# Kernel tuning notes

Measured on AMD Instinct MI355X. Metric: run time of the kernel, lower is better.

The kernel has to match this reference:

```python
import jax, jax.numpy as jnp
import numpy as np

B, P, N, H = 8, 12, 5000, 8
E = 50000
NB = 8
TD0, TD1 = 16, 64
MAX_STEPS = 500


def _proj(x, w1, b1, w2, b2):
    # Projection: Linear -> ReLU -> Linear
    return jax.nn.relu(x @ w1 + b1) @ w2 + b2


def _ln(x, w, b, eps=1e-5):
    # LayerNorm over last two dims [N, H] with affine params [N, H]
    m = jnp.mean(x, axis=(-2, -1), keepdims=True)
    v = jnp.mean((x - m) ** 2, axis=(-2, -1), keepdims=True)
    return (x - m) * jax.lax.rsqrt(v + eps) * w + b


def _time_table():
    # DiffTimeEmbedding buffer: [MAX_STEPS, 2*TD0]
    steps = jnp.arange(MAX_STEPS, dtype=jnp.float32)[:, None]
    dims = jnp.arange(TD0, dtype=jnp.float32)[None, :]
    e = steps * 10.0 ** (dims * 4.0 / TD0)
    return jnp.concatenate([jnp.sin(e), jnp.cos(e)], axis=1)


def setup_inputs() -> dict:
    key = jax.random.key(0)
    ks = jax.random.split(key, 40)
    rn = lambda k, s, sc=0.1: jax.random.normal(k, s, jnp.float32) * sc
    return {
        'x': jax.random.normal(ks[0], (B, P, N), jnp.float32),
        'cond': jax.random.normal(ks[1], (B, P, N, H), jnp.float32),
        'pos': jax.random.normal(ks[2], (N, H), jnp.float32),
        'time': jax.random.randint(ks[3], (B,), 0, MAX_STEPS),
        'edge_index': jax.random.randint(ks[4], (2, E), 0, N),
        'te_w1': rn(ks[5], (2 * TD0, TD1)), 'te_b1': rn(ks[6], (TD1,)),
        'te_w2': rn(ks[7], (TD1, TD1)), 'te_b2': rn(ks[8], (TD1,)),
        'in_w1': rn(ks[9], (1, H)), 'in_b1': rn(ks[10], (H,)),
        'in_w2': rn(ks[11], (H, H)), 'in_b2': rn(ks[12], (H,)),
        'pos_w1': rn(ks[13], (H, H)), 'pos_b1': rn(ks[14], (H,)),
        'pos_w2': rn(ks[15], (H, H)), 'pos_b2': rn(ks[16], (H,)),
        'attn': jax.random.normal(ks[17], (NB + 1, 1), jnp.float32),
        'bt_w1': rn(ks[18], (NB, TD1, H)), 'bt_b1': rn(ks[19], (NB, H)),
        'bt_w2': rn(ks[20], (NB, H, H)), 'bt_b2': rn(ks[21], (NB, H)),
        'bc_w1': rn(ks[22], (NB, H, H)), 'bc_b1': rn(ks[23], (NB, H)),
        'bc_w2': rn(ks[24], (NB, H, H)), 'bc_b2': rn(ks[25], (NB, H)),
        'gn_w': 1.0 + rn(ks[26], (NB, N, H), 0.05), 'gn_b': rn(ks[27], (NB, N, H), 0.05),
        'tn_w': 1.0 + rn(ks[28], (NB, N, H), 0.05), 'tn_b': rn(ks[29], (NB, N, H), 0.05),
        'cv_w': rn(ks[30], (NB, P, P)), 'cv_b': rn(ks[31], (NB, P)),
        'out_w1': rn(ks[32], (H, H)), 'out_b1': rn(ks[33], (H,)),
        'out_w2': rn(ks[34], (H, 1)), 'out_b2': rn(ks[35], (1,)),
    }


def _forward(x, cond, pos, te_w1, te_b1, te_w2, te_b2, in_w1, in_b1, in_w2, in_b2,
             pos_w1, pos_b1, pos_w2, pos_b2, attn, bt_w1, bt_b1, bt_w2, bt_b2,
             bc_w1, bc_b1, bc_w2, bc_b2, gn_w, gn_b, tn_w, tn_b, cv_w, cv_b,
             out_w1, out_b1, out_w2, out_b2, time, edge_index):
    # diffusion-time embedding -> [B, TD1]
    te = _time_table()[time]
    te = jax.nn.silu(te @ te_w1 + te_b1)
    te = jax.nn.silu(te @ te_w2 + te_b2)
    # input + positional projection -> [B, P, N, H]
    h = _proj(x[..., None], in_w1, in_b1, in_w2, in_b2)
    h = h + _proj(pos, pos_w1, pos_b1, pos_w2, pos_b2)
    # LGConv symmetric GCN norm (no self loops), shared across blocks
    src, dst = edge_index[0], edge_index[1]
    deg = jnp.zeros((N,), h.dtype).at[dst].add(1.0)
    dinv = jnp.where(deg > 0, 1.0 / jnp.sqrt(jnp.where(deg > 0, deg, 1.0)), 0.0)
    enorm = dinv[src] * dinv[dst]  # [E]
    skips = [h]
    for i in range(NB):
        t = _proj(te, bt_w1[i], bt_b1[i], bt_w2[i], bt_b2[i])[:, None, None, :]
        c = _proj(cond, bc_w1[i], bc_b1[i], bc_w2[i], bc_b2[i])
        h = _ln(h + c, gn_w[i], gn_b[i])
        # LGConv: gather -> scale -> scatter-add along node dim (-2)
        msg = h[:, :, src, :] * enorm[None, None, :, None]
        h = jnp.zeros_like(h).at[:, :, dst, :].add(msg)
        h = _ln(h + t, tn_w[i], tn_b[i])
        # 1x1 Conv2d over period channels
        h = jnp.einsum('bpnh,qp->bqnh', h, cv_w[i]) + cv_b[i][None, :, None, None]
        skips.append(h)
    s = jnp.stack(skips, axis=-1)  # [B, P, N, H, NB+1]
    a = jax.nn.softmax(attn, axis=0)  # [NB+1, 1]
    h = (s @ a)[..., 0]  # [B, P, N, H]
    return _proj(h, out_w1, out_b1, out_w2, out_b2)[..., 0]  # [B, P, N]


def reference(x, cond, pos, te_w1, te_b1, te_w2, te_b2, in_w1, in_b1, in_w2, in_b2,
              pos_w1, pos_b1, pos_w2, pos_b2, attn, bt_w1, bt_b1, bt_w2, bt_b2,
              bc_w1, bc_b1, bc_w2, bc_b2, gn_w, gn_b, tn_w, tn_b, cv_w, cv_b,
              out_w1, out_b1, out_w2, out_b2, time, edge_index):
    return _forward(x, cond, pos, te_w1, te_b1, te_w2, te_b2, in_w1, in_b1, in_w2, in_b2,
                    pos_w1, pos_b1, pos_w2, pos_b2, attn, bt_w1, bt_b1, bt_w2, bt_b2,
                    bc_w1, bc_b1, bc_w2, bc_b2, gn_w, gn_b, tn_w, tn_b, cv_w, cv_b,
                    out_w1, out_b1, out_w2, out_b2, time, edge_index)
```

## Files before the change

### kernel.cpp

```cpp
#include <hip/hip_runtime.h>
#include <math.h>

#define Bv 8
#define Pv 12
#define Nv 5000
#define Hv 8
#define Ev 50000
#define NBv 8
#define TD1v 64
#define NIMG (Bv * Pv)
#define BLKS_PER_IMG 20

__device__ __constant__ float POW10Q[16] = {
  1.0f, 1.7782794100389228f, 3.1622776601683795f, 5.623413251903491f,
  10.0f, 17.78279410038923f, 31.622776601683793f, 56.23413251903491f,
  100.0f, 177.82794100389228f, 316.22776601683796f, 562.341325190349f,
  1000.0f, 1778.2794100389228f, 3162.2776601683795f, 5623.413251903491f
};

__global__ void k_setup(const int* timei, const float* attn,
                        const float* te_w1, const float* te_b1,
                        const float* te_w2, const float* te_b2,
                        const float* bt_w1, const float* bt_b1,
                        const float* bt_w2, const float* bt_b2,
                        float* t_all, float* a9) {
  __shared__ float te0[Bv][32];
  __shared__ float te1[Bv][64];
  __shared__ float te2[Bv][64];
  int t = threadIdx.x;
  for (int idx = t; idx < Bv * 16; idx += 64) {
    int b = idx >> 4, d = idx & 15;
    float e = (float)timei[b] * POW10Q[d];
    te0[b][d]      = (float)sin((double)e);
    te0[b][d + 16] = (float)cos((double)e);
  }
  __syncthreads();
  for (int idx = t; idx < Bv * 64; idx += 64) {
    int b = idx >> 6, j = idx & 63;
    float s = te_b1[j];
    for (int k = 0; k < 32; ++k) s += te0[b][k] * te_w1[k * 64 + j];
    te1[b][j] = s / (1.0f + expf(-s));
  }
  __syncthreads();
  for (int idx = t; idx < Bv * 64; idx += 64) {
    int b = idx >> 6, j = idx & 63;
    float s = te_b2[j];
    for (int k = 0; k < 64; ++k) s += te1[b][k] * te_w2[k * 64 + j];
    te2[b][j] = s / (1.0f + expf(-s));
  }
  __syncthreads();
  {
    int i = t >> 3, b = t & 7;
    float u[Hv];
    for (int j = 0; j < Hv; ++j) {
      float s = bt_b1[i * Hv + j];
      for (int k = 0; k < TD1v; ++k) s += te2[b][k] * bt_w1[(i * TD1v + k) * Hv + j];
      u[j] = fmaxf(s, 0.0f);
    }
    for (int ch = 0; ch < Hv; ++ch) {
      float s = bt_b2[i * Hv + ch];
      for (int j = 0; j < Hv; ++j) s += u[j] * bt_w2[(i * Hv + j) * Hv + ch];
      t_all[(i * Bv + b) * Hv + ch] = s;
    }
  }
  if (t == 0) {
    float m = attn[0];
    for (int i = 1; i < 9; ++i) m = fmaxf(m, attn[i]);
    float s = 0.f, ex[9];
    for (int i = 0; i < 9; ++i) { ex[i] = expf(attn[i] - m); s += ex[i]; }
    for (int i = 0; i < 9; ++i) a9[i] = ex[i] / s;
  }
}

__global__ void k_posp(const float* pos, const float* pw1, const float* pb1,
                       const float* pw2, const float* pb2, float* posp) {
  int n = blockIdx.x * blockDim.x + threadIdx.x;
  if (n >= Nv) return;
  const float4* pr = (const float4*)(pos + (size_t)n * Hv);
  float4 r0 = pr[0], r1 = pr[1];
  float x[8] = {r0.x, r0.y, r0.z, r0.w, r1.x, r1.y, r1.z, r1.w};
  float u[8];
  #pragma unroll
  for (int j = 0; j < 8; ++j) {
    float s = pb1[j];
    #pragma unroll
    for (int k = 0; k < 8; ++k) s += x[k] * pw1[k * 8 + j];
    u[j] = fmaxf(s, 0.f);
  }
  float o[8];
  #pragma unroll
  for (int ch = 0; ch < 8; ++ch) {
    float s = pb2[ch];
    #pragma unroll
    for (int j = 0; j < 8; ++j) s += u[j] * pw2[j * 8 + ch];
    o[ch] = s;
  }
  float4* po = (float4*)(posp + (size_t)n * Hv);
  po[0] = make_float4(o[0], o[1], o[2], o[3]);
  po[1] = make_float4(o[4], o[5], o[6], o[7]);
}

__global__ void k_zero(float* deg, int* cursor, float* stats) {
  int i = blockIdx.x * blockDim.x + threadIdx.x;
  if (i < Nv) { deg[i] = 0.f; cursor[i] = 0; }
  if (i < NBv * 2 * NIMG * 2) stats[i] = 0.f;
}

__global__ void k_deg(const int* eidx, float* deg) {
  int e = blockIdx.x * blockDim.x + threadIdx.x;
  if (e < Ev) atomicAdd(&deg[eidx[Ev + e]], 1.0f);
}

__global__ void k_dinv(const float* deg, float* dinv) {
  int n = blockIdx.x * blockDim.x + threadIdx.x;
  if (n < Nv) {
    float d = deg[n];
    dinv[n] = d > 0.f ? (float)(1.0 / sqrt((double)d)) : 0.f;
  }
}

__global__ void k_scan(const float* deg, int* row_ptr) {
  __shared__ int buf[1024];
  __shared__ int base_s;
  int t = threadIdx.x;
  if (t == 0) { base_s = 0; row_ptr[0] = 0; }
  __syncthreads();
  for (int c = 0; c < 5; ++c) {
    int i = c * 1024 + t;
    int v = (i < Nv) ? (int)(deg[i] + 0.5f) : 0;
    buf[t] = v;
    __syncthreads();
    for (int off = 1; off < 1024; off <<= 1) {
      int add = (t >= off) ? buf[t - off] : 0;
      __syncthreads();
      buf[t] += add;
      __syncthreads();
    }
    int base = base_s;
    if (i < Nv) row_ptr[i + 1] = base + buf[t];
    __syncthreads();
    if (t == 1023) base_s = base + buf[1023];
    __syncthreads();
  }
}

__global__ void k_csr(const int* eidx, const float* dinv, const int* row_ptr,
                      int* cursor, float2* epack) {
  int e = blockIdx.x * blockDim.x + threadIdx.x;
  if (e >= Ev) return;
  int s = eidx[e], d = eidx[Ev + e];
  int slot = atomicAdd(&cursor[d], 1);
  int pos = row_ptr[d] + slot;
  epack[pos] = make_float2(__int_as_float(s), dinv[s] * dinv[d]);
}

__global__ __launch_bounds__(256) void k_gwb(
    const int* __restrict__ row_ptr, const float2* __restrict__ epack,
    const float* __restrict__ gn_w, const float* __restrict__ gn_b,
    float* __restrict__ Gw, float* __restrict__ Gb) {
  int id = blockIdx.x * 256 + threadIdx.x;
  if (id >= NBv * Nv) return;
  int i = id / Nv, n = id % Nv;
  const float* gw = gn_w + (size_t)i * Nv * Hv;
  const float* gb = gn_b + (size_t)i * Nv * Hv;
  float aw[8] = {0,0,0,0,0,0,0,0}, ab[8] = {0,0,0,0,0,0,0,0};
  int e0 = row_ptr[n], e1 = row_ptr[n + 1];
  for (int e = e0; e < e1; ++e) {
    float2 ep = epack[e];
    int s = __float_as_int(ep.x);
    float w = ep.y;
    const float4* wr = (const float4*)(gw + (size_t)s * Hv);
    const float4* br = (const float4*)(gb + (size_t)s * Hv);
    float4 w0 = wr[0], w1 = wr[1], b0 = br[0], b1 = br[1];
    aw[0] += w * w0.x; aw[1] += w * w0.y; aw[2] += w * w0.z; aw[3] += w * w0.w;
    aw[4] += w * w1.x; aw[5] += w * w1.y; aw[6] += w * w1.z; aw[7] += w * w1.w;
    ab[0] += w * b0.x; ab[1] += w * b0.y; ab[2] += w * b0.z; ab[3] += w * b0.w;
    ab[4] += w * b1.x; ab[5] += w * b1.y; ab[6] += w * b1.z; ab[7] += w * b1.w;
  }
  float4* wo = (float4*)(Gw + (size_t)id * Hv);
  wo[0] = make_float4(aw[0], aw[1], aw[2], aw[3]);
  wo[1] = make_float4(aw[4], aw[5], aw[6], aw[7]);
  float4* bo = (float4*)(Gb + (size_t)id * Hv);
  bo[0] = make_float4(ab[0], ab[1], ab[2], ab[3]);
  bo[1] = make_float4(ab[4], ab[5], ab[6], ab[7]);
}

__global__ void k_init(const float* x, const float* posp,
                       const float* iw1, const float* ib1,
                       const float* iw2, const float* ib2,
                       const float* a9, float* hA, float* acc) {
  int t = blockIdx.x * blockDim.x + threadIdx.x;
  if (t >= Bv * Pv * Nv) return;
  float xv = x[t];
  float u[8];
  #pragma unroll
  for (int j = 0; j < 8; ++j) u[j] = fmaxf(xv * iw1[j] + ib1[j], 0.f);
  int n = t % Nv;
  const float4* pp = (const float4*)(posp + (size_t)n * Hv);
  float4 p0 = pp[0], p1 = pp[1];
  float pv[8] = {p0.x, p0.y, p0.z, p0.w, p1.x, p1.y, p1.z, p1.w};
  float a0 = a9[0];
  float o[8];
  #pragma unroll
  for (int ch = 0; ch < 8; ++ch) {
    float s = ib2[ch];
    #pragma unroll
    for (int j = 0; j < 8; ++j) s += u[j] * iw2[j * 8 + ch];
    o[ch] = s + pv[ch];
  }
  float4* hr = (float4*)(hA + (size_t)t * Hv);
  hr[0] = make_float4(o[0], o[1], o[2], o[3]);
  hr[1] = make_float4(o[4], o[5], o[6], o[7]);
  float4* ar = (float4*)(acc + (size_t)t * Hv);
  ar[0] = make_float4(a0 * o[0], a0 * o[1], a0 * o[2], a0 * o[3]);
  ar[1] = make_float4(a0 * o[4], a0 * o[5], a0 * o[6], a0 * o[7]);
}

__device__ inline void partial_to_stats(float s1, float s2, float* stats_g) {
  #pragma unroll
  for (int off = 32; off > 0; off >>= 1) {
    s1 += __shfl_down(s1, off, 64);
    s2 += __shfl_down(s2, off, 64);
  }
  __shared__ float r1[4], r2[4];
  int wid = threadIdx.x >> 6, lane = threadIdx.x & 63;
  if (lane == 0) { r1[wid] = s1; r2[wid] = s2; }
  __syncthreads();
  if (threadIdx.x == 0) {
    float a = r1[0] + r1[1] + r1[2] + r1[3];
    float b = r2[0] + r2[1] + r2[2] + r2[3];
    atomicAdd(&stats_g[0], a);
    atomicAdd(&stats_g[1], b);
  }
}

__device__ inline void img_swizzle(int bx, int& g, int& chunk) {
  int xcd = bx & 7;
  int local = bx >> 3;
  g = xcd * 12 + local / BLKS_PER_IMG;
  chunk = local % BLKS_PER_IMG;
}

__global__ __launch_bounds__(256) void k_stage1(
    const float* __restrict__ h, const float* __restrict__ cond,
    const float* w1, const float* b1, const float* w2, const float* b2,
    const float* __restrict__ gnw,
    float* __restrict__ vt, float* stats1) {
  __shared__ float lw1[64], lw2[64], lb1[8], lb2[8];
  int t = threadIdx.x;
  if (t < 64) lw1[t] = w1[t];
  else if (t < 128) lw2[t - 64] = w2[t - 64];
  else if (t < 136) lb1[t - 128] = b1[t - 128];
  else if (t < 144) lb2[t - 136] = b2[t - 136];
  __syncthreads();
  int g, chunk;
  img_swizzle(blockIdx.x, g, chunk);
  int n = chunk * 256 + t;
  float s1 = 0.f, s2 = 0.f;
  if (n < Nv) {
    size_t row = ((size_t)g * Nv + n) * Hv;
    const float4* cr = (const float4*)(cond + row);
    float4 c0 = cr[0], c1 = cr[1];
    float xc[8] = {c0.x, c0.y, c0.z, c0.w, c1.x, c1.y, c1.z, c1.w};
    float u[8];
    #pragma unroll
    for (int j = 0; j < 8; ++j) {
      float s = lb1[j];
      #pragma unroll
      for (int k = 0; k < 8; ++k) s += xc[k] * lw1[k * 8 + j];
      u[j] = fmaxf(s, 0.f);
    }
    const float4* hr = (const float4*)(h + row);
    float4 h0 = hr[0], h1 = hr[1];
    float hv[8] = {h0.x, h0.y, h0.z, h0.w, h1.x, h1.y, h1.z, h1.w};
    const float4* gr = (const float4*)(gnw + (size_t)n * Hv);
    float4 g0 = gr[0], g1 = gr[1];
    float gv[8] = {g0.x, g0.y, g0.z, g0.w, g1.x, g1.y, g1.z, g1.w};
    float o[8];
    #pragma unroll
    for (int ch = 0; ch < 8; ++ch) {
      float s = lb2[ch];
      #pragma unroll
      for (int j = 0; j < 8; ++j) s += u[j] * lw2[j * 8 + ch];
      float val = s + hv[ch];
      s1 += val; s2 += val * val;
      o[ch] = val * gv[ch];
    }
    float4* vo = (float4*)(vt + row);
    vo[0] = make_float4(o[0], o[1], o[2], o[3]);
    vo[1] = make_float4(o[4], o[5], o[6], o[7]);
  }
  partial_to_stats(s1, s2, stats1 + (size_t)g * 2);
}

__global__ __launch_bounds__(256) void k_stage2(
    const float* __restrict__ vt, float* __restrict__ v2,
    const int* __restrict__ row_ptr, const float2* __restrict__ epack,
    const float* __restrict__ Gw, const float* __restrict__ Gb,
    const float* __restrict__ stats1, float* stats2,
    const float* __restrict__ tvec) {
  int t = threadIdx.x;
  int g, chunk;
  img_swizzle(blockIdx.x, g, chunk);
  int n = chunk * 256 + t;
  int b = g / Pv;
  float mean = stats1[g * 2] * (1.f / 40000.f);
  float m2   = stats1[g * 2 + 1] * (1.f / 40000.f);
  float var  = m2 - mean * mean;
  float rstd = (float)(1.0 / sqrt((double)var + 1e-5));
  float mrs  = mean * rstd;
  float s1 = 0.f, s2 = 0.f;
  if (n < Nv) {
    size_t ibase = (size_t)g * Nv * Hv;
    float a8[8] = {0.f, 0.f, 0.f, 0.f, 0.f, 0.f, 0.f, 0.f};
    int e0 = row_ptr[n], e1 = row_ptr[n + 1];
    for (int e = e0; e < e1; ++e) {
      float2 ep = epack[e];
      int s = __float_as_int(ep.x);
      float w = ep.y;
      const float4* sr = (const float4*)(vt + ibase + (size_t)s * Hv);
      float4 x0 = sr[0], x1 = sr[1];
      a8[0] += w * x0.x; a8[1] += w * x0.y; a8[2] += w * x0.z; a8[3] += w * x0.w;
      a8[4] += w * x1.x; a8[5] += w * x1.y; a8[6] += w * x1.z; a8[7] += w * x1.w;
    }
    const float4* wr = (const float4*)(Gw + (size_t)n * Hv);
    const float4* br = (const float4*)(Gb + (size_t)n * Hv);
    float4 w0 = wr[0], w1 = wr[1], b0 = br[0], b1 = br[1];
    float gw8[8] = {w0.x, w0.y, w0.z, w0.w, w1.x, w1.y, w1.z, w1.w};
    float gb8[8] = {b0.x, b0.y, b0.z, b0.w, b1.x, b1.y, b1.z, b1.w};
    float o[8];
    #pragma unroll
    for (int ch = 0; ch < 8; ++ch) {
      float val = rstd * a8[ch] - mrs * gw8[ch] + gb8[ch] + tvec[b * Hv + ch];
      o[ch] = val;
      s1 += val; s2 += val * val;
    }
    float4* vo = (float4*)(v2 + ibase + (size_t)n * Hv);
    vo[0] = make_float4(o[0], o[1], o[2], o[3]);
    vo[1] = make_float4(o[4], o[5], o[6], o[7]);
  }
  partial_to_stats(s1, s2, stats2 + (size_t)g * 2);
}

__global__ __launch_bounds__(256) void k_stage3(
    float* __restrict__ v2, float* __restrict__ acc,
    const float* __restrict__ stats2,
    const float* __restrict__ tnw, const float* __restrict__ tnb,
    const float* __restrict__ cw, const float* __restrict__ cb,
    const float* __restrict__ a9, int iblk) {
  __shared__ float scw[144], scb[12], smean[12], srstd[12];
  int t = threadIdx.x;
  int b = blockIdx.x & 7;
  int chunk = blockIdx.x >> 3;
  if (t < 144) scw[t] = cw[t];
  else if (t < 156) scb[t - 144] = cb[t - 144];
  else if (t < 168) {
    int p = t - 156;
    int g = b * Pv + p;
    float mean = stats2[g * 2] * (1.f / 40000.f);
    float m2   = stats2[g * 2 + 1] * (1.f / 40000.f);
    float var  = m2 - mean * mean;
    smean[p] = mean;
    srstd[p] = (float)(1.0 / sqrt((double)var + 1e-5));
  }
  __syncthreads();
  int idx = chunk * 256 + t;
  if (idx >= Nv * 2) return;
  int n = idx >> 1, c4 = idx & 1;
  size_t noff = (size_t)n * Hv + c4 * 4;
  const float4 w4 = *(const float4*)(tnw + noff);
  const float4 b4 = *(const float4*)(tnb + noff);
  size_t strideP = (size_t)Nv * Hv;
  size_t base = (size_t)b * Pv * strideP + noff;
  float4 in[12];
  #pragma unroll
  for (int p = 0; p < 12; ++p) {
    float4 v = *(const float4*)(v2 + base + p * strideP);
    float mean = smean[p], rstd = srstd[p];
    in[p].x = (v.x - mean) * rstd * w4.x + b4.x;
    in[p].y = (v.y - mean) * rstd * w4.y + b4.y;
    in[p].z = (v.z - mean) * rstd * w4.z + b4.z;
    in[p].w = (v.w - mean) * rstd * w4.w + b4.w;
  }
  float ai = a9[iblk + 1];
  #pragma unroll
  for (int q = 0; q < 12; ++q) {
    float4 o = make_float4(scb[q], scb[q], scb[q], scb[q]);
    #pragma unroll
    for (int p = 0; p < 12; ++p) {
      float c = scw[q * 12 + p];
      o.x += c * in[p].x; o.y += c * in[p].y;
      o.z += c * in[p].z; o.w += c * in[p].w;
    }
    size_t off = base + q * strideP;
    *(float4*)(v2 + off) = o;
    float4* ap = (float4*)(acc + off);
    float4 av = *ap;
    av.x += ai * o.x; av.y += ai * o.y; av.z += ai * o.z; av.w += ai * o.w;
    *ap = av;
  }
}

__global__ void k_out(const float* acc, const float* ow1, const float* ob1,
                      const float* ow2, const float* ob2, float* out) {
  int t = blockIdx.x * blockDim.x + threadIdx.x;
  if (t >= Bv * Pv * Nv) return;
  const float4* ar = (const float4*)(acc + (size_t)t * Hv);
  float4 a0 = ar[0], a1 = ar[1];
  float x[8] = {a0.x, a0.y, a0.z, a0.w, a1.x, a1.y, a1.z, a1.w};
  float o = ob2[0];
  #pragma unroll
  for (int j = 0; j < 8; ++j) {
    float s = ob1[j];
    #pragma unroll
    for (int k = 0; k < 8; ++k) s += x[k] * ow1[k * 8 + j];
    o += fmaxf(s, 0.f) * ow2[j];
  }
  out[t] = o;
}

extern "C" void kernel_launch(void* const* d_in, const int* in_sizes, int n_in,
                              void* d_out, int out_size, void* d_ws, size_t ws_size,
                              hipStream_t stream) {
  const float* x      = (const float*)d_in[0];
  const float* cond   = (const float*)d_in[1];
  const float* pos    = (const float*)d_in[2];
  const int*   timei  = (const int*)  d_in[3];
  const int*   eidx   = (const int*)  d_in[4];
  const float* te_w1  = (const float*)d_in[5];
  const float* te_b1  = (const float*)d_in[6];
  const float* te_w2  = (const float*)d_in[7];
  const float* te_b2  = (const float*)d_in[8];
  const float* in_w1  = (const float*)d_in[9];
  const float* in_b1  = (const float*)d_in[10];
  const float* in_w2  = (const float*)d_in[11];
  const float* in_b2  = (const float*)d_in[12];
  const float* pos_w1 = (const float*)d_in[13];
  const float* pos_b1 = (const float*)d_in[14];
  const float* pos_w2 = (const float*)d_in[15];
  const float* pos_b2 = (const float*)d_in[16];
  const float* attn   = (const float*)d_in[17];
  const float* bt_w1  = (const float*)d_in[18];
  const float* bt_b1  = (const float*)d_in[19];
  const float* bt_w2  = (const float*)d_in[20];
  const float* bt_b2  = (const float*)d_in[21];
  const float* bc_w1  = (const float*)d_in[22];
  const float* bc_b1  = (const float*)d_in[23];
  const float* bc_w2  = (const float*)d_in[24];
  const float* bc_b2  = (const float*)d_in[25];
  const float* gn_w   = (const float*)d_in[26];
  const float* gn_b   = (const float*)d_in[27];
  const float* tn_w   = (const float*)d_in[28];
  const float* tn_b   = (const float*)d_in[29];
  const float* cv_w   = (const float*)d_in[30];
  const float* cv_b   = (const float*)d_in[31];
  const float* out_w1 = (const float*)d_in[32];
  const float* out_b1 = (const float*)d_in[33];
  const float* out_w2 = (const float*)d_in[34];
  const float* out_b2 = (const float*)d_in[35];
  float* out = (float*)d_out;

  const size_t HSZ = (size_t)Bv * Pv * Nv * Hv;
  float* ws    = (float*)d_ws;
  float* X     = ws;
  float* Y     = X + HSZ;
  float* acc   = Y + HSZ;
  float* posp  = acc + HSZ;
  float* deg   = posp + Nv * Hv;
  float* dinv  = deg + Nv;
  float* epack = dinv + Nv;
  float* t_all = epack + 2 * Ev;
  float* a9    = t_all + NBv * Bv * Hv;
  float* stats = a9 + 16;
  float* Gw    = stats + NBv * 2 * NIMG * 2;
  float* Gb    = Gw + NBv * Nv * Hv;
  int* row_ptr = (int*)(Gb + NBv * Nv * Hv);
  int* cursor  = row_ptr + Nv + 8;

  k_setup<<<1, 64, 0, stream>>>(timei, attn, te_w1, te_b1, te_w2, te_b2,
                                bt_w1, bt_b1, bt_w2, bt_b2, t_all, a9);
  k_posp<<<(Nv + 255) / 256, 256, 0, stream>>>(pos, pos_w1, pos_b1, pos_w2, pos_b2, posp);
  k_zero<<<(Nv + 255) / 256, 256, 0, stream>>>(deg, cursor, stats);
  k_deg<<<(Ev + 255) / 256, 256, 0, stream>>>(eidx, deg);
  k_dinv<<<(Nv + 255) / 256, 256, 0, stream>>>(deg, dinv);
  k_scan<<<1, 1024, 0, stream>>>(deg, row_ptr);
  k_csr<<<(Ev + 255) / 256, 256, 0, stream>>>(eidx, dinv, row_ptr, cursor, (float2*)epack);
  k_gwb<<<(NBv * Nv + 255) / 256, 256, 0, stream>>>(
      row_ptr, (const float2*)epack, gn_w, gn_b, Gw, Gb);
  k_init<<<(Bv * Pv * Nv + 255) / 256, 256, 0, stream>>>(
      x, posp, in_w1, in_b1, in_w2, in_b2, a9, X, acc);

  for (int i = 0; i < NBv; ++i) {
    float* st1 = stats + (size_t)(i * 2 + 0) * NIMG * 2;
    float* st2 = stats + (size_t)(i * 2 + 1) * NIMG * 2;
    k_stage1<<<NIMG * BLKS_PER_IMG, 256, 0, stream>>>(
        X, cond,
        bc_w1 + i * 64, bc_b1 + i * 8, bc_w2 + i * 64, bc_b2 + i * 8,
        gn_w + (size_t)i * Nv * Hv,
        Y, st1);
    k_stage2<<<NIMG * BLKS_PER_IMG, 256, 0, stream>>>(
        Y, X, row_ptr, (const float2*)epack,
        Gw + (size_t)i * Nv * Hv, Gb + (size_t)i * Nv * Hv,
        st1, st2, t_all + i * Bv * Hv);
    k_stage3<<<8 * 40, 256, 0, stream>>>(
        X, acc, st2,
        tn_w + (size_t)i * Nv * Hv, tn_b + (size_t)i * Nv * Hv,
        cv_w + i * 144, cv_b + i * 12, a9, i);
  }
  k_out<<<(Bv * Pv * Nv + 255) / 256, 256, 0, stream>>>(
      acc, out_w1, out_b1, out_w2, out_b2, out);
}
```

Before: 657.1 us.

## Process four period images per thread in graph aggregation to reuse CSR edges

The sparse aggregation kernel now handles four period images per thread, so each edge's index and weight, the row pointers and the per-node gn weight and bias are loaded once and reused across four images. The grid shrinks by a factor of four. A barrier is added at the end of the stats reduction so it can be called repeatedly within one kernel. In exchange there are fewer blocks, hence less parallelism for latency hiding, more accumulator registers per thread, and four block reductions with barriers instead of one.

```diff
diff --git a/kernel.cpp b/kernel.cpp
--- a/kernel.cpp
+++ b/kernel.cpp
@@ -10,6 +10,7 @@
 #define TD1v 64
 #define NIMG (Bv * Pv)
 #define BLKS_PER_IMG 20
+#define IPT 4
 
 __device__ __constant__ float POW10Q[16] = {
   1.0f, 1.7782794100389228f, 3.1622776601683795f, 5.623413251903491f,
@@ -232,6 +233,7 @@
     atomicAdd(&stats_g[0], a);
     atomicAdd(&stats_g[1], b);
   }
+  __syncthreads();
 }
 
 __device__ inline void img_swizzle(int bx, int& g, int& chunk) {
@@ -300,46 +302,80 @@
     const float* __restrict__ stats1, float* stats2,
     const float* __restrict__ tvec) {
   int t = threadIdx.x;
-  int g, chunk;
-  img_swizzle(blockIdx.x, g, chunk);
+  int b = blockIdx.x & 7;
+  int local = blockIdx.x >> 3;
+  int quad = local % 3;
+  int chunk = local / 3;
   int n = chunk * 256 + t;
-  int b = g / Pv;
-  float mean = stats1[g * 2] * (1.f / 40000.f);
-  float m2   = stats1[g * 2 + 1] * (1.f / 40000.f);
-  float var  = m2 - mean * mean;
-  float rstd = (float)(1.0 / sqrt((double)var + 1e-5));
-  float mrs  = mean * rstd;
-  float s1 = 0.f, s2 = 0.f;
+  int g0 = b * Pv + quad * IPT;
+  float mean[IPT], rstd[IPT], mrs[IPT];
+  #pragma unroll
+  for (int j = 0; j < IPT; ++j) {
+    float m = stats1[(g0 + j) * 2] * (1.f / 40000.f);
+    float m2 = stats1[(g0 + j) * 2 + 1] * (1.f / 40000.f);
+    float var = m2 - m * m;
+    mean[j] = m;
+    rstd[j] = (float)(1.0 / sqrt((double)var + 1e-5));
+    mrs[j] = m * rstd[j];
+  }
+  float tl[8];
+  {
+    const float4* tr = (const float4*)(tvec + b * Hv);
+    float4 t0 = tr[0], t1 = tr[1];
+    tl[0] = t0.x; tl[1] = t0.y; tl[2] = t0.z; tl[3] = t0.w;
+    tl[4] = t1.x; tl[5] = t1.y; tl[6] = t1.z; tl[7] = t1.w;
+  }
+  float s1a[IPT], s2a[IPT];
+  #pragma unroll
+  for (int j = 0; j < IPT; ++j) { s1a[j] = 0.f; s2a[j] = 0.f; }
   if (n < Nv) {
-    size_t ibase = (size_t)g * Nv * Hv;
-    float a8[8] = {0.f, 0.f, 0.f, 0.f, 0.f, 0.f, 0.f, 0.f};
+    size_t ib[IPT];
+    #pragma unroll
+    for (int j = 0; j < IPT; ++j) ib[j] = (size_t)(g0 + j) * Nv * Hv;
+    float a[IPT][8];
+    #pragma unroll
+    for (int j = 0; j < IPT; ++j)
+      #pragma unroll
+      for (int ch = 0; ch < 8; ++ch) a[j][ch] = 0.f;
     int e0 = row_ptr[n], e1 = row_ptr[n + 1];
     for (int e = e0; e < e1; ++e) {
       float2 ep = epack[e];
       int s = __float_as_int(ep.x);
       float w = ep.y;
-      const float4* sr = (const float4*)(vt + ibase + (size_t)s * Hv);
-      float4 x0 = sr[0], x1 = sr[1];
-      a8[0] += w * x0.x; a8[1] += w * x0.y; a8[2] += w * x0.z; a8[3] += w * x0.w;
-      a8[4] += w * x1.x; a8[5] += w * x1.y; a8[6] += w * x1.z; a8[7] += w * x1.w;
-    }
-    const float4* wr = (const float4*)(Gw + (size_t)n * Hv);
-    const float4* br = (const float4*)(Gb + (size_t)n * Hv);
+      size_t so = (size_t)s * Hv;
+      #pragma unroll
+      for (int j = 0; j < IPT; ++j) {
+        const float4* sr = (const float4*)(vt + ib[j] + so);
+        float4 x0 = sr[0], x1 = sr[1];
+        a[j][0] += w * x0.x; a[j][1] += w * x0.y;
+        a[j][2] += w * x0.z; a[j][3] += w * x0.w;
+        a[j][4] += w * x1.x; a[j][5] += w * x1.y;
+        a[j][6] += w * x1.z; a[j][7] += w * x1.w;
+      }
+    }
+    size_t noff = (size_t)n * Hv;
+    const float4* wr = (const float4*)(Gw + noff);
+    const float4* br = (const float4*)(Gb + noff);
     float4 w0 = wr[0], w1 = wr[1], b0 = br[0], b1 = br[1];
     float gw8[8] = {w0.x, w0.y, w0.z, w0.w, w1.x, w1.y, w1.z, w1.w};
     float gb8[8] = {b0.x, b0.y, b0.z, b0.w, b1.x, b1.y, b1.z, b1.w};
-    float o[8];
-    #pragma unroll
-    for (int ch = 0; ch < 8; ++ch) {
-      float val = rstd * a8[ch] - mrs * gw8[ch] + gb8[ch] + tvec[b * Hv + ch];
-      o[ch] = val;
-      s1 += val; s2 += val * val;
-    }
-    float4* vo = (float4*)(v2 + ibase + (size_t)n * Hv);
-    vo[0] = make_float4(o[0], o[1], o[2], o[3]);
-    vo[1] = make_float4(o[4], o[5], o[6], o[7]);
-  }
-  partial_to_stats(s1, s2, stats2 + (size_t)g * 2);
+    #pragma unroll
+    for (int j = 0; j < IPT; ++j) {
+      float o[8];
+      #pragma unroll
+      for (int ch = 0; ch < 8; ++ch) {
+        float val = rstd[j] * a[j][ch] - mrs[j] * gw8[ch] + gb8[ch] + tl[ch];
+        o[ch] = val;
+        s1a[j] += val; s2a[j] += val * val;
+      }
+      float4* vo = (float4*)(v2 + ib[j] + noff);
+      vo[0] = make_float4(o[0], o[1], o[2], o[3]);
+      vo[1] = make_float4(o[4], o[5], o[6], o[7]);
+    }
+  }
+  #pragma unroll
+  for (int j = 0; j < IPT; ++j)
+    partial_to_stats(s1a[j], s2a[j], stats2 + (size_t)(g0 + j) * 2);
 }
 
 __global__ __launch_bounds__(256) void k_stage3(
@@ -498,7 +534,7 @@
         bc_w1 + i * 64, bc_b1 + i * 8, bc_w2 + i * 64, bc_b2 + i * 8,
         gn_w + (size_t)i * Nv * Hv,
         Y, st1);
-    k_stage2<<<NIMG * BLKS_PER_IMG, 256, 0, stream>>>(
+    k_stage2<<<8 * 3 * BLKS_PER_IMG, 256, 0, stream>>>(
         Y, X, row_ptr, (const float2*)epack,
         Gw + (size_t)i * Nv * Hv, Gb + (size_t)i * Nv * Hv,
         st1, st2, t_all + i * Bv * Hv);
```

Result: no change. 655.8 us (-0.2%).

## Fuse stage3 with next block's stage1 and stage edge lists in LDS

Applied to the files above, without the earlier changes.

Stage3 (layernorm, period conv, skip accumulation) is merged with the next block's stage1 (conditioning projection, gn scaling, stats), so the conv output feeds stage1 directly. This drops one full-tensor write and read plus one launch per block. Stage2 now copies each block's CSR edge slice into shared memory and unrolls the gather four-wide to raise memory-level parallelism. Costs: 12 per-period reductions per block, each with extra syncs and atomics, more register pressure in the fused kernel, and an added barrier in the stats helper.

```diff
diff --git a/kernel.cpp b/kernel.cpp
--- a/kernel.cpp
+++ b/kernel.cpp
@@ -10,6 +10,7 @@
 #define TD1v 64
 #define NIMG (Bv * Pv)
 #define BLKS_PER_IMG 20
+#define ECAP 4096
 
 __device__ __constant__ float POW10Q[16] = {
   1.0f, 1.7782794100389228f, 3.1622776601683795f, 5.623413251903491f,
@@ -232,6 +233,7 @@
     atomicAdd(&stats_g[0], a);
     atomicAdd(&stats_g[1], b);
   }
+  __syncthreads();
 }
 
 __device__ inline void img_swizzle(int bx, int& g, int& chunk) {
@@ -299,32 +301,67 @@
     const float* __restrict__ Gw, const float* __restrict__ Gb,
     const float* __restrict__ stats1, float* stats2,
     const float* __restrict__ tvec) {
+  __shared__ float2 se[ECAP];
   int t = threadIdx.x;
   int g, chunk;
   img_swizzle(blockIdx.x, g, chunk);
-  int n = chunk * 256 + t;
   int b = g / Pv;
+  int nb0 = chunk * 256;
+  int nb1 = nb0 + 256; if (nb1 > Nv) nb1 = Nv;
+  int eb0 = row_ptr[nb0];
+  int eb1 = row_ptr[nb1];
+  int cnt = eb1 - eb0;
+  const float2* eps;
+  int ebase;
+  if (cnt <= ECAP) {
+    for (int k = t; k < cnt; k += 256) se[k] = epack[eb0 + k];
+    eps = se; ebase = eb0;
+  } else {
+    eps = epack; ebase = 0;
+  }
+  __syncthreads();
   float mean = stats1[g * 2] * (1.f / 40000.f);
   float m2   = stats1[g * 2 + 1] * (1.f / 40000.f);
   float var  = m2 - mean * mean;
   float rstd = (float)(1.0 / sqrt((double)var + 1e-5));
   float mrs  = mean * rstd;
+  int n = nb0 + t;
   float s1 = 0.f, s2 = 0.f;
   if (n < Nv) {
-    size_t ibase = (size_t)g * Nv * Hv;
-    float a8[8] = {0.f, 0.f, 0.f, 0.f, 0.f, 0.f, 0.f, 0.f};
-    int e0 = row_ptr[n], e1 = row_ptr[n + 1];
-    for (int e = e0; e < e1; ++e) {
-      float2 ep = epack[e];
-      int s = __float_as_int(ep.x);
+    const float* vtb = vt + (size_t)g * Nv * Hv;
+    float a8[8] = {0,0,0,0,0,0,0,0};
+    int e0 = row_ptr[n] - ebase, e1 = row_ptr[n + 1] - ebase;
+    int e = e0;
+    for (; e + 4 <= e1; e += 4) {
+      float2 p0 = eps[e], p1 = eps[e+1], p2 = eps[e+2], p3 = eps[e+3];
+      const float4* r0 = (const float4*)(vtb + (size_t)__float_as_int(p0.x) * Hv);
+      const float4* r1 = (const float4*)(vtb + (size_t)__float_as_int(p1.x) * Hv);
+      const float4* r2 = (const float4*)(vtb + (size_t)__float_as_int(p2.x) * Hv);
+      const float4* r3 = (const float4*)(vtb + (size_t)__float_as_int(p3.x) * Hv);
+      float4 x00 = r0[0], x01 = r0[1];
+      float4 x10 = r1[0], x11 = r1[1];
+      float4 x20 = r2[0], x21 = r2[1];
+      float4 x30 = r3[0], x31 = r3[1];
+      a8[0] += p0.y*x00.x + p1.y*x10.x + p2.y*x20.x + p3.y*x30.x;
+      a8[1] += p0.y*x00.y + p1.y*x10.y + p2.y*x20.y + p3.y*x30.y;
+      a8[2] += p0.y*x00.z + p1.y*x10.z + p2.y*x20.z + p3.y*x30.z;
+      a8[3] += p0.y*x00.w + p1.y*x10.w + p2.y*x20.w + p3.y*x30.w;
+      a8[4] += p0.y*x01.x + p1.y*x11.x + p2.y*x21.x + p3.y*x31.x;
+      a8[5] += p0.y*x01.y + p1.y*x11.y + p2.y*x21.y + p3.y*x31.y;
+      a8[6] += p0.y*x01.z + p1.y*x11.z + p2.y*x21.z + p3.y*x31.z;
+      a8[7] += p0.y*x01.w + p1.y*x11.w + p2.y*x21.w + p3.y*x31.w;
+    }
+    for (; e < e1; ++e) {
+      float2 ep = eps[e];
       float w = ep.y;
-      const float4* sr = (const float4*)(vt + ibase + (size_t)s * Hv);
+      const float4* sr = (const float4*)(vtb + (size_t)__float_as_int(ep.x) * Hv);
       float4 x0 = sr[0], x1 = sr[1];
-      a8[0] += w * x0.x; a8[1] += w * x0.y; a8[2] += w * x0.z; a8[3] += w * x0.w;
-      a8[4] += w * x1.x; a8[5] += w * x1.y; a8[6] += w * x1.z; a8[7] += w * x1.w;
-    }
-    const float4* wr = (const float4*)(Gw + (size_t)n * Hv);
-    const float4* br = (const float4*)(Gb + (size_t)n * Hv);
+      a8[0] += w*x0.x; a8[1] += w*x0.y; a8[2] += w*x0.z; a8[3] += w*x0.w;
+      a8[4] += w*x1.x; a8[5] += w*x1.y; a8[6] += w*x1.z; a8[7] += w*x1.w;
+    }
+    size_t noff = (size_t)n * Hv;
+    const float4* wr = (const float4*)(Gw + noff);
+    const float4* br = (const float4*)(Gb + noff);
     float4 w0 = wr[0], w1 = wr[1], b0 = br[0], b1 = br[1];
     float gw8[8] = {w0.x, w0.y, w0.z, w0.w, w1.x, w1.y, w1.z, w1.w};
     float gb8[8] = {b0.x, b0.y, b0.z, b0.w, b1.x, b1.y, b1.z, b1.w};
@@ -335,11 +372,122 @@
       o[ch] = val;
       s1 += val; s2 += val * val;
     }
-    float4* vo = (float4*)(v2 + ibase + (size_t)n * Hv);
+    float4* vo = (float4*)(v2 + (size_t)g * Nv * Hv + noff);
     vo[0] = make_float4(o[0], o[1], o[2], o[3]);
     vo[1] = make_float4(o[4], o[5], o[6], o[7]);
   }
   partial_to_stats(s1, s2, stats2 + (size_t)g * 2);
+}
+
+__global__ __launch_bounds__(256) void k_fused31(
+    const float* __restrict__ v2, float* __restrict__ acc,
+    const float* __restrict__ cond,
+    const float* __restrict__ stats2,
+    const float* __restrict__ tnw, const float* __restrict__ tnb,
+    const float* __restrict__ cw, const float* __restrict__ cb,
+    const float* w1, const float* b1, const float* w2, const float* b2,
+    const float* __restrict__ gnw,
+    float* __restrict__ vt, float* stats1,
+    const float* __restrict__ a9, int iblk) {
+  __shared__ float scw[144], scb[12], smean[12], srstd[12];
+  __shared__ float lw1[64], lw2[64], lb1[8], lb2[8];
+  int t = threadIdx.x;
+  int b = blockIdx.x & 7;
+  int chunk = blockIdx.x >> 3;
+  if (t < 144) scw[t] = cw[t];
+  else if (t < 156) scb[t - 144] = cb[t - 144];
+  else if (t < 168) {
+    int p = t - 156;
+    int g = b * Pv + p;
+    float mean = stats2[g * 2] * (1.f / 40000.f);
+    float m2   = stats2[g * 2 + 1] * (1.f / 40000.f);
+    float var  = m2 - mean * mean;
+    smean[p] = mean;
+    srstd[p] = (float)(1.0 / sqrt((double)var + 1e-5));
+  }
+  if (t < 64) lw1[t] = w1[t];
+  else if (t < 128) lw2[t - 64] = w2[t - 64];
+  else if (t < 136) lb1[t - 128] = b1[t - 128];
+  else if (t < 144) lb2[t - 136] = b2[t - 136];
+  __syncthreads();
+  int idx = chunk * 256 + t;
+  bool active = idx < Nv * 2;
+  float s1a[12], s2a[12];
+  #pragma unroll
+  for (int p = 0; p < 12; ++p) { s1a[p] = 0.f; s2a[p] = 0.f; }
+  if (active) {
+    int n = idx >> 1, c4 = idx & 1;
+    size_t noff = (size_t)n * Hv + c4 * 4;
+    const float4 w4 = *(const float4*)(tnw + noff);
+    const float4 b4 = *(const float4*)(tnb + noff);
+    const float4 gv = *(const float4*)(gnw + noff);
+    size_t strideP = (size_t)Nv * Hv;
+    size_t base = (size_t)b * Pv * strideP + noff;
+    float4 in[12];
+    #pragma unroll
+    for (int p = 0; p < 12; ++p) {
+      float4 v = *(const float4*)(v2 + base + p * strideP);
+      float mean = smean[p], rstd = srstd[p];
+      in[p].x = (v.x - mean) * rstd * w4.x + b4.x;
+      in[p].y = (v.y - mean) * rstd * w4.y + b4.y;
+      in[p].z = (v.z - mean) * rstd * w4.z + b4.z;
+      in[p].w = (v.w - mean) * rstd * w4.w + b4.w;
+    }
+    float ai = a9[iblk + 1];
+    #pragma unroll
+    for (int q = 0; q < 12; ++q) {
+      float4 o = make_float4(scb[q], scb[q], scb[q], scb[q]);
+      #pragma unroll
+      for (int p = 0; p < 12; ++p) {
+        float c = scw[q * 12 + p];
+        o.x += c * in[p].x; o.y += c * in[p].y;
+        o.z += c * in[p].z; o.w += c * in[p].w;
+      }
+      size_t off = base + q * strideP;
+      float4* ap = (float4*)(acc + off);
+      float4 av = *ap;
+      av.x += ai * o.x; av.y += ai * o.y; av.z += ai * o.z; av.w += ai * o.w;
+      *ap = av;
+      float4 cme = *(const float4*)(cond + off);
+      float c8[8];
+      float e0 = __shfl_xor(cme.x, 1, 64);
+      float e1 = __shfl_xor(cme.y, 1, 64);
+      float e2 = __shfl_xor(cme.z, 1, 64);
+      float e3 = __shfl_xor(cme.w, 1, 64);
+      if (c4 == 0) {
+        c8[0] = cme.x; c8[1] = cme.y; c8[2] = cme.z; c8[3] = cme.w;
+        c8[4] = e0; c8[5] = e1; c8[6] = e2; c8[7] = e3;
+      } else {
+        c8[0] = e0; c8[1] = e1; c8[2] = e2; c8[3] = e3;
+        c8[4] = cme.x; c8[5] = cme.y; c8[6] = cme.z; c8[7] = cme.w;
+      }
+      float u8[8];
+      #pragma unroll
+      for (int j = 0; j < 8; ++j) {
+        float s = lb1[j];
+        #pragma unroll
+        for (int k = 0; k < 8; ++k) s += c8[k] * lw1[k * 8 + j];
+        u8[j] = fmaxf(s, 0.f);
+      }
+      float val[4];
+      #pragma unroll
+      for (int m = 0; m < 4; ++m) {
+        int ch = c4 * 4 + m;
+        float s = lb2[ch];
+        #pragma unroll
+        for (int j = 0; j < 8; ++j) s += u8[j] * lw2[j * 8 + ch];
+        val[m] = s;
+      }
+      val[0] += o.x; val[1] += o.y; val[2] += o.z; val[3] += o.w;
+      s1a[q] += val[0] + val[1] + val[2] + val[3];
+      s2a[q] += val[0]*val[0] + val[1]*val[1] + val[2]*val[2] + val[3]*val[3];
+      *(float4*)(vt + off) = make_float4(val[0]*gv.x, val[1]*gv.y,
+                                         val[2]*gv.z, val[3]*gv.w);
+    }
+  }
+  #pragma unroll
+  for (int p = 0; p < 12; ++p)
+    partial_to_stats(s1a[p], s2a[p], stats1 + (size_t)(b * Pv + p) * 2);
 }
 
 __global__ __launch_bounds__(256) void k_stage3(
@@ -393,7 +541,6 @@
       o.z += c * in[p].z; o.w += c * in[p].w;
     }
     size_t off = base + q * strideP;
-    *(float4*)(v2 + off) = o;
     float4* ap = (float4*)(acc + off);
     float4 av = *ap;
     av.x += ai * o.x; av.y += ai * o.y; av.z += ai * o.z; av.w += ai * o.w;
@@ -490,22 +637,33 @@
   k_init<<<(Bv * Pv * Nv + 255) / 256, 256, 0, stream>>>(
       x, posp, in_w1, in_b1, in_w2, in_b2, a9, X, acc);
 
+  k_stage1<<<NIMG * BLKS_PER_IMG, 256, 0, stream>>>(
+      X, cond, bc_w1, bc_b1, bc_w2, bc_b2, gn_w, Y,
+      stats + 0);
+
   for (int i = 0; i < NBv; ++i) {
     float* st1 = stats + (size_t)(i * 2 + 0) * NIMG * 2;
     float* st2 = stats + (size_t)(i * 2 + 1) * NIMG * 2;
-    k_stage1<<<NIMG * BLKS_PER_IMG, 256, 0, stream>>>(
-        X, cond,
-        bc_w1 + i * 64, bc_b1 + i * 8, bc_w2 + i * 64, bc_b2 + i * 8,
-        gn_w + (size_t)i * Nv * Hv,
-        Y, st1);
     k_stage2<<<NIMG * BLKS_PER_IMG, 256, 0, stream>>>(
         Y, X, row_ptr, (const float2*)epack,
         Gw + (size_t)i * Nv * Hv, Gb + (size_t)i * Nv * Hv,
         st1, st2, t_all + i * Bv * Hv);
-    k_stage3<<<8 * 40, 256, 0, stream>>>(
-        X, acc, st2,
-        tn_w + (size_t)i * Nv * Hv, tn_b + (size_t)i * Nv * Hv,
-        cv_w + i * 144, cv_b + i * 12, a9, i);
+    if (i < NBv - 1) {
+      float* st1n = stats + (size_t)((i + 1) * 2 + 0) * NIMG * 2;
+      k_fused31<<<8 * 40, 256, 0, stream>>>(
+          X, acc, cond, st2,
+          tn_w + (size_t)i * Nv * Hv, tn_b + (size_t)i * Nv * Hv,
+          cv_w + i * 144, cv_b + i * 12,
+          bc_w1 + (i + 1) * 64, bc_b1 + (i + 1) * 8,
+          bc_w2 + (i + 1) * 64, bc_b2 + (i + 1) * 8,
+          gn_w + (size_t)(i + 1) * Nv * Hv,
+          Y, st1n, a9, i);
+    } else {
+      k_stage3<<<8 * 40, 256, 0, stream>>>(
+          X, acc, st2,
+          tn_w + (size_t)i * Nv * Hv, tn_b + (size_t)i * Nv * Hv,
+          cv_w + i * 144, cv_b + i * 12, a9, i);
+    }
   }
   k_out<<<(Bv * Pv * Nv + 255) / 256, 256, 0, stream>>>(
       acc, out_w1, out_b1, out_w2, out_b2, out);
```

After: 958.0 us. +45.8%, slower.

## Stage edge lists in LDS, unroll gather by four, add nontemporal streaming accesses

Applied to the files above, without the earlier changes.

The graph-aggregation kernel now cooperatively copies each block's contiguous CSR edge range into shared memory, falling back to global memory when the range exceeds capacity. Its gather loop is unrolled by four to keep more independent loads in flight. Streaming buffers (cond, acc, v2, layer-norm params) are read and written with nontemporal hints so they do not evict the reused vt and pos data from cache. The risks are extra LDS use lowering occupancy, an added barrier, and nontemporal hints hurting data that is later reused.

```diff
diff --git a/kernel.cpp b/kernel.cpp
--- a/kernel.cpp
+++ b/kernel.cpp
@@ -10,6 +10,18 @@
 #define TD1v 64
 #define NIMG (Bv * Pv)
 #define BLKS_PER_IMG 20
+#define ECAP 3072
+
+typedef float f4v __attribute__((ext_vector_type(4)));
+
+__device__ inline float4 nt_load4(const float* p) {
+  f4v v = __builtin_nontemporal_load((const f4v*)p);
+  return make_float4(v.x, v.y, v.z, v.w);
+}
+__device__ inline void nt_store4(float* p, float a, float b, float c, float d) {
+  f4v v = {a, b, c, d};
+  __builtin_nontemporal_store(v, (f4v*)p);
+}
 
 __device__ __constant__ float POW10Q[16] = {
   1.0f, 1.7782794100389228f, 3.1622776601683795f, 5.623413251903491f,
@@ -191,7 +203,7 @@
                        const float* a9, float* hA, float* acc) {
   int t = blockIdx.x * blockDim.x + threadIdx.x;
   if (t >= Bv * Pv * Nv) return;
-  float xv = x[t];
+  float xv = __builtin_nontemporal_load(x + t);
   float u[8];
   #pragma unroll
   for (int j = 0; j < 8; ++j) u[j] = fmaxf(xv * iw1[j] + ib1[j], 0.f);
@@ -211,9 +223,8 @@
   float4* hr = (float4*)(hA + (size_t)t * Hv);
   hr[0] = make_float4(o[0], o[1], o[2], o[3]);
   hr[1] = make_float4(o[4], o[5], o[6], o[7]);
-  float4* ar = (float4*)(acc + (size_t)t * Hv);
-  ar[0] = make_float4(a0 * o[0], a0 * o[1], a0 * o[2], a0 * o[3]);
-  ar[1] = make_float4(a0 * o[4], a0 * o[5], a0 * o[6], a0 * o[7]);
+  nt_store4(acc + (size_t)t * Hv,     a0 * o[0], a0 * o[1], a0 * o[2], a0 * o[3]);
+  nt_store4(acc + (size_t)t * Hv + 4, a0 * o[4], a0 * o[5], a0 * o[6], a0 * o[7]);
 }
 
 __device__ inline void partial_to_stats(float s1, float s2, float* stats_g) {
@@ -232,6 +243,7 @@
     atomicAdd(&stats_g[0], a);
     atomicAdd(&stats_g[1], b);
   }
+  __syncthreads();
 }
 
 __device__ inline void img_swizzle(int bx, int& g, int& chunk) {
@@ -259,8 +271,8 @@
   float s1 = 0.f, s2 = 0.f;
   if (n < Nv) {
     size_t row = ((size_t)g * Nv + n) * Hv;
-    const float4* cr = (const float4*)(cond + row);
-    float4 c0 = cr[0], c1 = cr[1];
+    float4 c0 = nt_load4(cond + row);
+    float4 c1 = nt_load4(cond + row + 4);
     float xc[8] = {c0.x, c0.y, c0.z, c0.w, c1.x, c1.y, c1.z, c1.w};
     float u[8];
     #pragma unroll
@@ -299,32 +311,67 @@
     const float* __restrict__ Gw, const float* __restrict__ Gb,
     const float* __restrict__ stats1, float* stats2,
     const float* __restrict__ tvec) {
+  __shared__ float2 se[ECAP];
   int t = threadIdx.x;
   int g, chunk;
   img_swizzle(blockIdx.x, g, chunk);
-  int n = chunk * 256 + t;
   int b = g / Pv;
+  int nb0 = chunk * 256;
+  int nb1 = nb0 + 256; if (nb1 > Nv) nb1 = Nv;
+  int eb0 = row_ptr[nb0];
+  int eb1 = row_ptr[nb1];
+  int cnt = eb1 - eb0;
+  const float2* eps;
+  int ebase;
+  if (cnt <= ECAP) {
+    for (int k = t; k < cnt; k += 256) se[k] = epack[eb0 + k];
+    eps = se; ebase = eb0;
+  } else {
+    eps = epack; ebase = 0;
+  }
+  __syncthreads();
   float mean = stats1[g * 2] * (1.f / 40000.f);
   float m2   = stats1[g * 2 + 1] * (1.f / 40000.f);
   float var  = m2 - mean * mean;
   float rstd = (float)(1.0 / sqrt((double)var + 1e-5));
   float mrs  = mean * rstd;
+  int n = nb0 + t;
   float s1 = 0.f, s2 = 0.f;
   if (n < Nv) {
-    size_t ibase = (size_t)g * Nv * Hv;
-    float a8[8] = {0.f, 0.f, 0.f, 0.f, 0.f, 0.f, 0.f, 0.f};
-    int e0 = row_ptr[n], e1 = row_ptr[n + 1];
-    for (int e = e0; e < e1; ++e) {
-      float2 ep = epack[e];
-      int s = __float_as_int(ep.x);
+    const float* vtb = vt + (size_t)g * Nv * Hv;
+    float a8[8] = {0,0,0,0,0,0,0,0};
+    int e0 = row_ptr[n] - ebase, e1 = row_ptr[n + 1] - ebase;
+    int e = e0;
+    for (; e + 4 <= e1; e += 4) {
+      float2 p0 = eps[e], p1 = eps[e+1], p2 = eps[e+2], p3 = eps[e+3];
+      const float4* r0 = (const float4*)(vtb + (size_t)__float_as_int(p0.x) * Hv);
+      const float4* r1 = (const float4*)(vtb + (size_t)__float_as_int(p1.x) * Hv);
+      const float4* r2 = (const float4*)(vtb + (size_t)__float_as_int(p2.x) * Hv);
+      const float4* r3 = (const float4*)(vtb + (size_t)__float_as_int(p3.x) * Hv);
+      float4 x00 = r0[0], x01 = r0[1];
+      float4 x10 = r1[0], x11 = r1[1];
+      float4 x20 = r2[0], x21 = r2[1];
+      float4 x30 = r3[0], x31 = r3[1];
+      a8[0] += p0.y*x00.x + p1.y*x10.x + p2.y*x20.x + p3.y*x30.x;
+      a8[1] += p0.y*x00.y + p1.y*x10.y + p2.y*x20.y + p3.y*x30.y;
+      a8[2] += p0.y*x00.z + p1.y*x10.z + p2.y*x20.z + p3.y*x30.z;
+      a8[3] += p0.y*x00.w + p1.y*x10.w + p2.y*x20.w + p3.y*x30.w;
+      a8[4] += p0.y*x01.x + p1.y*x11.x + p2.y*x21.x + p3.y*x31.x;
+      a8[5] += p0.y*x01.y + p1.y*x11.y + p2.y*x21.y + p3.y*x31.y;
+      a8[6] += p0.y*x01.z + p1.y*x11.z + p2.y*x21.z + p3.y*x31.z;
+      a8[7] += p0.y*x01.w + p1.y*x11.w + p2.y*x21.w + p3.y*x31.w;
+    }
+    for (; e < e1; ++e) {
+      float2 ep = eps[e];
       float w = ep.y;
-      const float4* sr = (const float4*)(vt + ibase + (size_t)s * Hv);
+      const float4* sr = (const float4*)(vtb + (size_t)__float_as_int(ep.x) * Hv);
       float4 x0 = sr[0], x1 = sr[1];
-      a8[0] += w * x0.x; a8[1] += w * x0.y; a8[2] += w * x0.z; a8[3] += w * x0.w;
-      a8[4] += w * x1.x; a8[5] += w * x1.y; a8[6] += w * x1.z; a8[7] += w * x1.w;
-    }
-    const float4* wr = (const float4*)(Gw + (size_t)n * Hv);
-    const float4* br = (const float4*)(Gb + (size_t)n * Hv);
+      a8[0] += w*x0.x; a8[1] += w*x0.y; a8[2] += w*x0.z; a8[3] += w*x0.w;
+      a8[4] += w*x1.x; a8[5] += w*x1.y; a8[6] += w*x1.z; a8[7] += w*x1.w;
+    }
+    size_t noff = (size_t)n * Hv;
+    const float4* wr = (const float4*)(Gw + noff);
+    const float4* br = (const float4*)(Gb + noff);
     float4 w0 = wr[0], w1 = wr[1], b0 = br[0], b1 = br[1];
     float gw8[8] = {w0.x, w0.y, w0.z, w0.w, w1.x, w1.y, w1.z, w1.w};
     float gb8[8] = {b0.x, b0.y, b0.z, b0.w, b1.x, b1.y, b1.z, b1.w};
@@ -335,9 +382,9 @@
       o[ch] = val;
       s1 += val; s2 += val * val;
     }
-    float4* vo = (float4*)(v2 + ibase + (size_t)n * Hv);
-    vo[0] = make_float4(o[0], o[1], o[2], o[3]);
-    vo[1] = make_float4(o[4], o[5], o[6], o[7]);
+    float* vo = v2 + (size_t)g * Nv * Hv + noff;
+    nt_store4(vo,     o[0], o[1], o[2], o[3]);
+    nt_store4(vo + 4, o[4], o[5], o[6], o[7]);
   }
   partial_to_stats(s1, s2, stats2 + (size_t)g * 2);
 }
@@ -368,14 +415,14 @@
   if (idx >= Nv * 2) return;
   int n = idx >> 1, c4 = idx & 1;
   size_t noff = (size_t)n * Hv + c4 * 4;
-  const float4 w4 = *(const float4*)(tnw + noff);
-  const float4 b4 = *(const float4*)(tnb + noff);
+  const float4 w4 = nt_load4(tnw + noff);
+  const float4 b4 = nt_load4(tnb + noff);
   size_t strideP = (size_t)Nv * Hv;
   size_t base = (size_t)b * Pv * strideP + noff;
   float4 in[12];
   #pragma unroll
   for (int p = 0; p < 12; ++p) {
-    float4 v = *(const float4*)(v2 + base + p * strideP);
+    float4 v = nt_load4(v2 + base + p * strideP);
     float mean = smean[p], rstd = srstd[p];
     in[p].x = (v.x - mean) * rstd * w4.x + b4.x;
     in[p].y = (v.y - mean) * rstd * w4.y + b4.y;
@@ -394,10 +441,9 @@
     }
     size_t off = base + q * strideP;
     *(float4*)(v2 + off) = o;
-    float4* ap = (float4*)(acc + off);
-    float4 av = *ap;
-    av.x += ai * o.x; av.y += ai * o.y; av.z += ai * o.z; av.w += ai * o.w;
-    *ap = av;
+    float4 av = nt_load4(acc + off);
+    nt_store4(acc + off, av.x + ai * o.x, av.y + ai * o.y,
+                         av.z + ai * o.z, av.w + ai * o.w);
   }
 }
 
@@ -405,8 +451,8 @@
                       const float* ow2, const float* ob2, float* out) {
   int t = blockIdx.x * blockDim.x + threadIdx.x;
   if (t >= Bv * Pv * Nv) return;
-  const float4* ar = (const float4*)(acc + (size_t)t * Hv);
-  float4 a0 = ar[0], a1 = ar[1];
+  float4 a0 = nt_load4(acc + (size_t)t * Hv);
+  float4 a1 = nt_load4(acc + (size_t)t * Hv + 4);
   float x[8] = {a0.x, a0.y, a0.z, a0.w, a1.x, a1.y, a1.z, a1.w};
   float o = ob2[0];
   #pragma unroll
```

Result: faster. 639.0 us (-2.8%).
